# Kernel optimization log

Measured on AMD Instinct MI355X. Metric: run time of the kernel, lower is better.

The kernel has to match this reference:

```python
import jax, jax.numpy as jnp
import numpy as np

N = 64
D_MODEL = 512
L_MAX = 2048
BATCH = 8
DT_MIN, DT_MAX = 1e-3, 1e-1


def _make_s4_buffers(n):
    r = np.arange(1, n + 1, dtype=np.float64)
    # hippo[i,j] = sqrt(2(i+1)+1)*sqrt(2(j+1)+1) if i>j, (i+1)+1 on diag, else 0
    hippo = np.where(r[:, None] > r[None, :],
                     np.sqrt(2 * r[:, None] + 1.0) * np.sqrt(2 * r[None, :] + 1.0),
                     0.0)
    hippo = hippo + np.diag(r + 1.0)
    nhippo = -hippo
    p = 0.5 * np.sqrt(2.0 * r + 1.0)
    q = 2.0 * p
    S = nhippo + p[:, None] * q[None, :]
    lmbda, V = np.linalg.eig(S)
    Vc = V.conj().T
    p = Vc @ p
    q = Vc @ q.conj()
    return (p.astype(np.complex64), q.astype(np.complex64), lmbda.astype(np.complex64))


def setup_inputs() -> dict:
    key = jax.random.key(0)
    ku, kb, kc, ks = jax.random.split(key, 4)
    u = jax.random.normal(ku, (BATCH, L_MAX, D_MODEL), dtype=jnp.float32)
    std = float(np.sqrt(2.0 / (N + D_MODEL)))  # xavier_normal for (n, d_model)
    B = jax.random.normal(kb, (D_MODEL, N), dtype=jnp.float32) * std
    Ct = jax.random.normal(kc, (D_MODEL, N), dtype=jnp.float32) * std
    D = jnp.ones((D_MODEL,), dtype=jnp.float32)
    scale = float(np.log(DT_MAX) - np.log(DT_MIN))
    log_step = jax.random.uniform(ks, (D_MODEL,), dtype=jnp.float32) * scale + float(np.log(DT_MIN))
    p, q, lmbda = _make_s4_buffers(N)
    omega_l = np.exp(2j * np.pi / L_MAX * np.arange(L_MAX)).astype(np.complex64)
    return {"u": u, "B": B, "Ct": Ct, "D": D, "log_step": log_step,
            "p": jnp.asarray(p), "q": jnp.asarray(q), "lmbda": jnp.asarray(lmbda),
            "omega_l": jnp.asarray(omega_l)}


def _s4_kernel(B, Ct, log_step, p, q, lmbda, omega_l):
    L = omega_l.shape[0]
    step = jnp.exp(log_step)                                   # [d]
    g = jnp.outer(2.0 / step, (1.0 - omega_l) / (1.0 + omega_l))  # [d, L] complex
    c = 2.0 / (1.0 + omega_l)                                  # [L]
    # shared Cauchy resolvent: 1/(g - lambda), [d, L, n]
    r = 1.0 / (g[:, :, None] - lmbda)
    a0 = jnp.conj(Ct)  # [d, n]
    a1 = jnp.conj(q)   # [n]
    k00 = jnp.einsum('dn,dln->dl', a0 * B, r)
    k01 = jnp.einsum('dn,dln->dl', a0 * p, r)
    k10 = jnp.einsum('dn,dln->dl', a1 * B, r)
    k11 = jnp.einsum('n,dln->dl', a1 * p, r)
    at_roots = c * (k00 - k01 * (1.0 / (1.0 + k11)) * k10)     # [d, L]
    Kf = jnp.fft.ifft(at_roots, n=L, axis=-1)
    order = (-jnp.arange(L)) % L                               # [0, L-1, ..., 1]
    return Kf[:, order].real                                   # [d, L] float32


def reference(u, B, Ct, D, log_step, p, q, lmbda, omega_l):
    L = u.shape[1]
    K = _s4_kernel(B, Ct, log_step, p, q, lmbda, omega_l)      # [d, L]
    # non-circular FFT convolution
    ud = jnp.fft.rfft(jnp.pad(u, ((0, 0), (0, L), (0, 0))), axis=1)   # [B, L+1, d]
    Kd = jnp.fft.rfft(jnp.pad(K, ((0, 0), (0, L))), axis=-1)          # [d, L+1]
    y = jnp.fft.irfft(ud.transpose(0, 2, 1) * Kd, axis=-1)[..., :L]   # [B, d, L]
    return y.transpose(0, 2, 1) + D[None, None, :] * u
```

## Files before the change

### kernel.cpp

```cpp
#include <hip/hip_runtime.h>
#include <hip/hip_bf16.h>

#define NT 256
#define R2f 0.70710678118654752f
#define CS1 0.92387953251128674f
#define SN1 0.38268343236508978f
#define PI2 6.2831853071795865f

__device__ __forceinline__ float2 cmulf(float2 a, float2 b) {
    return make_float2(a.x * b.x - a.y * b.y, a.x * b.y + a.y * b.x);
}
__device__ __forceinline__ float2 cadd(float2 a, float2 b) { return make_float2(a.x + b.x, a.y + b.y); }
__device__ __forceinline__ float2 csub(float2 a, float2 b) { return make_float2(a.x - b.x, a.y - b.y); }

template<bool INV>
__device__ __forceinline__ float2 tww(float2 v, float wx, float wy) {
    float sy = INV ? -wy : wy;
    return make_float2(v.x * wx - v.y * sy, v.x * sy + v.y * wx);
}
template<bool INV>
__device__ __forceinline__ float2 mul_mi(float2 v) {
    return INV ? make_float2(-v.y, v.x) : make_float2(v.y, -v.x);
}

template<bool INV>
__device__ __forceinline__ void dft4(float2& a, float2& b, float2& c, float2& d) {
    float2 t0 = cadd(a, c), t1 = csub(a, c);
    float2 t2 = cadd(b, d), t3 = csub(b, d);
    float2 jt3 = mul_mi<INV>(t3);
    a = cadd(t0, t2);
    c = csub(t0, t2);
    b = cadd(t1, jt3);
    d = csub(t1, jt3);
}

template<bool INV>
__device__ __forceinline__ void fft16_tail(float2 v[16]) {
    v[5]  = tww<INV>(v[5],  CS1, -SN1);
    v[9]  = tww<INV>(v[9],  R2f, -R2f);
    v[13] = tww<INV>(v[13], SN1, -CS1);
    v[6]  = tww<INV>(v[6],  R2f, -R2f);
    v[10] = mul_mi<INV>(v[10]);
    v[14] = tww<INV>(v[14], -R2f, -R2f);
    v[7]  = tww<INV>(v[7],  SN1, -CS1);
    v[11] = tww<INV>(v[11], -R2f, -R2f);
    v[15] = tww<INV>(v[15], -CS1,  SN1);
    dft4<INV>(v[0],  v[1],  v[2],  v[3]);
    dft4<INV>(v[4],  v[5],  v[6],  v[7]);
    dft4<INV>(v[8],  v[9],  v[10], v[11]);
    dft4<INV>(v[12], v[13], v[14], v[15]);
    float2 t;
    t = v[1];  v[1]  = v[4];  v[4]  = t;
    t = v[2];  v[2]  = v[8];  v[8]  = t;
    t = v[3];  v[3]  = v[12]; v[12] = t;
    t = v[6];  v[6]  = v[9];  v[9]  = t;
    t = v[7];  v[7]  = v[13]; v[13] = t;
    t = v[11]; v[11] = v[14]; v[14] = t;
}

template<bool INV>
__device__ __forceinline__ void fft16(float2 v[16]) {
    dft4<INV>(v[0], v[4], v[8],  v[12]);
    dft4<INV>(v[1], v[5], v[9],  v[13]);
    dft4<INV>(v[2], v[6], v[10], v[14]);
    dft4<INV>(v[3], v[7], v[11], v[15]);
    fft16_tail<INV>(v);
}

__device__ __forceinline__ void fft16_hz(float2 v[16]) {
    #pragma unroll
    for (int i = 0; i < 4; ++i) {
        float2 a = v[i], b = v[i + 4];
        float2 jb = make_float2(b.y, -b.x);
        v[i]      = cadd(a, b);
        v[i + 4]  = cadd(a, jb);
        v[i + 8]  = csub(a, b);
        v[i + 12] = csub(a, jb);
    }
    fft16_tail<false>(v);
}

template<bool INV>
__device__ __forceinline__ void twchain(float2 v[16], float ang) {
    float s, c;
    __sincosf(INV ? ang : -ang, &s, &c);
    float2 w = make_float2(c, s);
    float2 t = w;
    v[1] = cmulf(v[1], t);
    #pragma unroll
    for (int a = 2; a < 16; ++a) { t = cmulf(t, w); v[a] = cmulf(v[a], t); }
}

template<bool INV>
__device__ void fft4096(float2 v[16], float2* lds, int tid) {
    const int hi = tid >> 4, lo = tid & 15;
    if (!INV) {
        fft16_hz(v);
        twchain<false>(v, PI2 * (float)tid * (1.0f / 4096.0f));
        __syncthreads();
        #pragma unroll
        for (int a = 0; a < 16; ++a) lds[tid + 256 * a] = v[a];
        __syncthreads();
        #pragma unroll
        for (int m1 = 0; m1 < 16; ++m1) v[m1] = lds[(m1 * 16 + lo) + 256 * hi];
        fft16<false>(v);
        twchain<false>(v, PI2 * (float)lo * (1.0f / 256.0f));
        __syncthreads();
        #pragma unroll
        for (int b = 0; b < 16; ++b) { int e = lo + 16 * b + 256 * hi; lds[e ^ b] = v[b]; }
        __syncthreads();
        #pragma unroll
        for (int m0 = 0; m0 < 16; ++m0) { int e = m0 + 16 * lo + 256 * hi; v[m0] = lds[e ^ lo]; }
        fft16<false>(v);
    } else {
        fft16<true>(v);
        __syncthreads();
        #pragma unroll
        for (int m0 = 0; m0 < 16; ++m0) { int e = m0 + 16 * lo + 256 * hi; lds[e ^ lo] = v[m0]; }
        __syncthreads();
        #pragma unroll
        for (int b = 0; b < 16; ++b) { int e = lo + 16 * b + 256 * hi; v[b] = lds[e ^ b]; }
        twchain<true>(v, PI2 * (float)lo * (1.0f / 256.0f));
        fft16<true>(v);
        __syncthreads();
        #pragma unroll
        for (int m1 = 0; m1 < 16; ++m1) lds[(m1 * 16 + lo) + 256 * hi] = v[m1];
        __syncthreads();
        #pragma unroll
        for (int a = 0; a < 16; ++a) v[a] = lds[tid + 256 * a];
        twchain<true>(v, PI2 * (float)tid * (1.0f / 4096.0f));
        fft16<true>(v);
    }
}

__global__ __launch_bounds__(256) void cauchy_kernel(
    const float* __restrict__ Bmat, const float* __restrict__ Ct,
    const float* __restrict__ log_step,
    const float2* __restrict__ p, const float2* __restrict__ q,
    const float2* __restrict__ lmbda, const float2* __restrict__ omega,
    float2* __restrict__ at)
{
    __shared__ float4 wA[64];
    __shared__ float4 wB[64];
    const int tid = threadIdx.x;
    const int d = blockIdx.x >> 2;
    const int lbase = (blockIdx.x & 3) << 8;

    if (tid < 64) {
        float b  = Bmat[d * 64 + tid];
        float ct = Ct[d * 64 + tid];
        float2 pp = p[tid], qq = q[tid];
        float2 lam = lmbda[tid];
        wA[tid] = make_float4(lam.x, lam.y, ct * b, qq.x * pp.x + qq.y * pp.y);
        wB[tid] = make_float4(ct * pp.x, ct * pp.y, b * qq.x, b * qq.y);
    }
    __syncthreads();

    const float two_over_dt = 2.0f * __expf(-log_step[d]);
    float2* atd = at + ((size_t)d << 11);

    const int l = lbase + tid;
    float2 om = omega[l];
    float dnx = 1.0f + om.x, dny = om.y;
    float id2 = __builtin_amdgcn_rcpf(dnx * dnx + dny * dny);
    float ivx = dnx * id2, ivy = -dny * id2;
    float ccx = 2.0f * ivx, ccy = 2.0f * ivy;
    float nmx = 1.0f - om.x, nmy = -om.y;
    float gx = two_over_dt * (nmx * ivx - nmy * ivy);
    float gy = two_over_dt * (nmx * ivy + nmy * ivx);

    float S00x = 0.f, S00y = 0.f, Sax = 0.f, Say = 0.f, Sbx = 0.f, Sby = 0.f;
    float Scx = 0.f, Scy = 0.f, Sdx = 0.f, Sdy = 0.f, S11x = 0.f, S11y = 0.f;

    #pragma unroll 8
    for (int n = 0; n < 64; ++n) {
        float4 A  = wA[n];
        float4 Bw = wB[n];
        float dx  = gx - A.x;
        float dy  = gy - A.y;
        float ir  = __builtin_amdgcn_rcpf(fmaf(dx, dx, dy * dy));
        float rx  = dx * ir;
        float ry  = -dy * ir;
        S00x = fmaf(A.z,  rx, S00x); S00y = fmaf(A.z,  ry, S00y);
        S11x = fmaf(A.w,  rx, S11x); S11y = fmaf(A.w,  ry, S11y);
        Sax  = fmaf(Bw.x, rx, Sax);  Say  = fmaf(Bw.x, ry, Say);
        Sbx  = fmaf(Bw.y, rx, Sbx);  Sby  = fmaf(Bw.y, ry, Sby);
        Scx  = fmaf(Bw.z, rx, Scx);  Scy  = fmaf(Bw.z, ry, Scy);
        Sdx  = fmaf(Bw.w, rx, Sdx);  Sdy  = fmaf(Bw.w, ry, Sdy);
    }

    {
        float k01x = Sax - Sby, k01y = Say + Sbx;
        float k10x = Scx + Sdy, k10y = Scy - Sdx;
        float ntx = k01x * k10x - k01y * k10y;
        float nty = k01x * k10y + k01y * k10x;
        float ox = 1.0f + S11x, oy = S11y;
        float oid = __builtin_amdgcn_rcpf(ox * ox + oy * oy);
        float tx = (ntx * ox + nty * oy) * oid;
        float ty = (nty * ox - ntx * oy) * oid;
        float inx = S00x - tx, iny = S00y - ty;
        float2 val = make_float2(ccx * inx - ccy * iny, ccx * iny + ccy * inx);
        atd[l] = val;
        if (l != 0) atd[2048 - l] = make_float2(val.x, -val.y);
    }

    if ((blockIdx.x & 3) == 3 && tid == 0) {
        float2 om1 = omega[1024];
        float dnx1 = 1.0f + om1.x, dny1 = om1.y;
        float id21 = __builtin_amdgcn_rcpf(dnx1 * dnx1 + dny1 * dny1);
        float ivx1 = dnx1 * id21, ivy1 = -dny1 * id21;
        float cx = 2.0f * ivx1, cy = 2.0f * ivy1;
        float nmx1 = 1.0f - om1.x, nmy1 = -om1.y;
        float ggx = two_over_dt * (nmx1 * ivx1 - nmy1 * ivy1);
        float ggy = two_over_dt * (nmx1 * ivy1 + nmy1 * ivx1);
        float s00x = 0.f, s00y = 0.f, sax = 0.f, say = 0.f, sbx = 0.f, sby = 0.f;
        float scx = 0.f, scy = 0.f, sdx = 0.f, sdy = 0.f, s11x = 0.f, s11y = 0.f;
        for (int n = 0; n < 64; ++n) {
            float4 A  = wA[n];
            float4 Bw = wB[n];
            float dx  = ggx - A.x;
            float dy  = ggy - A.y;
            float ir  = __builtin_amdgcn_rcpf(fmaf(dx, dx, dy * dy));
            float rx  = dx * ir;
            float ry  = -dy * ir;
            s00x = fmaf(A.z,  rx, s00x); s00y = fmaf(A.z,  ry, s00y);
            s11x = fmaf(A.w,  rx, s11x); s11y = fmaf(A.w,  ry, s11y);
            sax  = fmaf(Bw.x, rx, sax);  say  = fmaf(Bw.x, ry, say);
            sbx  = fmaf(Bw.y, rx, sbx);  sby  = fmaf(Bw.y, ry, sby);
            scx  = fmaf(Bw.z, rx, scx);  scy  = fmaf(Bw.z, ry, scy);
            sdx  = fmaf(Bw.w, rx, sdx);  sdy  = fmaf(Bw.w, ry, sdy);
        }
        float k01x = sax - sby, k01y = say + sbx;
        float k10x = scx + sdy, k10y = scy - sdx;
        float ntx = k01x * k10x - k01y * k10y;
        float nty = k01x * k10y + k01y * k10x;
        float ox = 1.0f + s11x, oy = s11y;
        float oid = __builtin_amdgcn_rcpf(ox * ox + oy * oy);
        float tx = (ntx * ox + nty * oy) * oid;
        float ty = (nty * ox - ntx * oy) * oid;
        float inx = s00x - tx, iny = s00y - ty;
        atd[1024] = make_float2(cx * inx - cy * iny, cx * iny + cy * inx);
    }
}

__global__ __launch_bounds__(256) void transpose_pack_kernel(
    const float* __restrict__ u, float2* __restrict__ z)
{
    __shared__ float2 tile[64][33];
    const int tid = threadIdx.x;
    int sub = blockIdx.x;
    int lt = sub & 63;
    int dt = (sub >> 6) & 7;
    int bp = sub >> 9;
    const size_t ub0 = (size_t)(2 * bp) * 2048 * 512;
    const size_t ub1 = (size_t)(2 * bp + 1) * 2048 * 512;
    #pragma unroll
    for (int r = 0; r < 8; ++r) {
        int idx = tid + 256 * r;
        int l_in = idx >> 6;
        int d_in = idx & 63;
        size_t off = (size_t)(lt * 32 + l_in) * 512 + (dt * 64 + d_in);
        tile[d_in][l_in] = make_float2(u[ub0 + off], u[ub1 + off]);
    }
    __syncthreads();
    #pragma unroll
    for (int r = 0; r < 8; ++r) {
        int idx = tid + 256 * r;
        int d_out = idx >> 5;
        int l_out = idx & 31;
        z[((size_t)(bp * 512 + dt * 64 + d_out)) * 2048 + lt * 32 + l_out] = tile[d_out][l_out];
    }
}

__global__ __launch_bounds__(256) void khat_kernel(
    const float2* __restrict__ at, float2* __restrict__ Khat)
{
    __shared__ float2 lds[4096];
    const int tid = threadIdx.x;
    const int d = blockIdx.x;
    const int hi = tid >> 4, lo = tid & 15;
    float2 v[16];

    const float2* ap = at + ((size_t)d << 11);
    #pragma unroll
    for (int n2 = 0; n2 < 8; ++n2) v[n2] = ap[tid + 256 * n2];
    #pragma unroll
    for (int n2 = 8; n2 < 16; ++n2) v[n2] = make_float2(0.f, 0.f);

    fft4096<false>(v, lds, tid);

    float* ldsf = (float*)lds;
    __syncthreads();
    if (!(hi & 1)) {
        int a2 = hi >> 1;
        #pragma unroll
        for (int c = 0; c < 16; ++c) {
            int j = 128 * c + 8 * lo + a2;
            ldsf[j ^ ((j >> 5) & 3)] = v[c].x * (1.0f / (2048.0f * 4096.0f));
        }
    }
    __syncthreads();
    #pragma unroll
    for (int n2 = 0; n2 < 8; ++n2) {
        int j = tid + 256 * n2;
        v[n2] = make_float2(ldsf[j ^ ((j >> 5) & 3)], 0.f);
    }
    #pragma unroll
    for (int n2 = 8; n2 < 16; ++n2) v[n2] = make_float2(0.f, 0.f);

    fft4096<false>(v, lds, tid);

    float2* op = Khat + ((size_t)d << 12);
    #pragma unroll
    for (int c = 0; c < 16; ++c) op[c * 256 + tid] = v[c];
}

__global__ __launch_bounds__(256) void conv_kernel(
    float2* __restrict__ z, const float2* __restrict__ Khat,
    const float* __restrict__ D)
{
    __shared__ float2 lds[4096];
    const int tid = threadIdx.x;
    const int d  = blockIdx.x & 511;
    const int bp = blockIdx.x >> 9;
    float2 v[16];
    float2 u0[8];

    float2* zr = z + ((size_t)(bp * 512 + d)) * 2048;
    #pragma unroll
    for (int n2 = 0; n2 < 8; ++n2) { u0[n2] = zr[tid + 256 * n2]; v[n2] = u0[n2]; }
    #pragma unroll
    for (int n2 = 8; n2 < 16; ++n2) v[n2] = make_float2(0.f, 0.f);

    fft4096<false>(v, lds, tid);

    const float2* kh = Khat + ((size_t)d << 12);
    #pragma unroll
    for (int c = 0; c < 16; ++c) v[c] = cmulf(v[c], kh[c * 256 + tid]);

    fft4096<true>(v, lds, tid);

    const float Dd = D[d];
    #pragma unroll
    for (int n2 = 0; n2 < 8; ++n2) {
        zr[tid + 256 * n2] =
            make_float2(v[n2].x + Dd * u0[n2].x, v[n2].y + Dd * u0[n2].y);
    }
}

__global__ __launch_bounds__(256) void untranspose_kernel(
    const float2* __restrict__ yz, float* __restrict__ out)
{
    __shared__ float2 tile[64][65];
    int blk = blockIdx.x;
    int lt  = blk & 31;
    int dt8 = (blk >> 5) & 7;
    int bp  = blk >> 8;
    for (int r = 0; r < 16; ++r) {
        int idx = threadIdx.x + 256 * r;
        int row = idx >> 6;
        int col = idx & 63;
        float2 vv = yz[((size_t)(bp * 512 + dt8 * 64 + row)) * 2048 + lt * 64 + col];
        tile[col][row] = vv;
    }
    __syncthreads();
    const size_t ub0 = (size_t)(2 * bp) * 2048 * 512;
    const size_t ub1 = (size_t)(2 * bp + 1) * 2048 * 512;
    for (int r = 0; r < 16; ++r) {
        int idx = threadIdx.x + 256 * r;
        int row = idx >> 6;
        int col = idx & 63;
        size_t off = (size_t)(lt * 64 + row) * 512 + (dt8 * 64 + col);
        float2 vv = tile[row][col];
        out[ub0 + off] = vv.x;
        out[ub1 + off] = vv.y;
    }
}

extern "C" void kernel_launch(void* const* d_in, const int* in_sizes, int n_in,
                              void* d_out, int out_size, void* d_ws, size_t ws_size,
                              hipStream_t stream) {
    (void)in_sizes; (void)n_in; (void)out_size; (void)ws_size;
    const float*  u   = (const float*)d_in[0];
    const float*  Bm  = (const float*)d_in[1];
    const float*  Ct  = (const float*)d_in[2];
    const float*  D   = (const float*)d_in[3];
    const float*  ls  = (const float*)d_in[4];
    const float2* p   = (const float2*)d_in[5];
    const float2* q   = (const float2*)d_in[6];
    const float2* lm  = (const float2*)d_in[7];
    const float2* om  = (const float2*)d_in[8];
    float* out = (float*)d_out;

    float2* Khat = (float2*)d_ws;
    float2* z    = (float2*)((char*)d_ws + (size_t)512 * 4096 * 8);
    float2* at   = z;

    hipLaunchKernelGGL(cauchy_kernel, dim3(2048), dim3(256), 0, stream,
                       Bm, Ct, ls, p, q, lm, om, at);
    hipLaunchKernelGGL(khat_kernel, dim3(512), dim3(256), 0, stream, at, Khat);
    hipLaunchKernelGGL(transpose_pack_kernel, dim3(2048), dim3(256), 0, stream, u, z);
    hipLaunchKernelGGL(conv_kernel, dim3(2048), dim3(256), 0, stream, z, Khat, D);
    hipLaunchKernelGGL(untranspose_kernel, dim3(1024), dim3(256), 0, stream, z, out);
}
```

Baseline: 93.64 us.

## Split FFT LDS exchanges into real/imag passes with padding to shrink shared memory

The 4096-point FFT now stages data through LDS as separate real and imaginary float passes in a padded float buffer (about 17 KB instead of 32 KB). This roughly halves per-block LDS so more conv blocks can be resident per CU, and padding is meant to cut bank conflicts. The khat kernel is restructured into 1024-thread blocks that each handle four d channels with their own LDS slices. The cost is twice as many __syncthreads and LDS round trips per transpose, and block-wide barriers in khat now span four independent FFTs.

```diff
diff --git a/kernel.cpp b/kernel.cpp
--- a/kernel.cpp
+++ b/kernel.cpp
@@ -6,12 +6,14 @@
 #define CS1 0.92387953251128674f
 #define SN1 0.38268343236508978f
 #define PI2 6.2831853071795865f
+#define LDSN 4336
 
 __device__ __forceinline__ float2 cmulf(float2 a, float2 b) {
     return make_float2(a.x * b.x - a.y * b.y, a.x * b.y + a.y * b.x);
 }
 __device__ __forceinline__ float2 cadd(float2 a, float2 b) { return make_float2(a.x + b.x, a.y + b.y); }
 __device__ __forceinline__ float2 csub(float2 a, float2 b) { return make_float2(a.x - b.x, a.y - b.y); }
+__device__ __forceinline__ int padx(int i) { return i + ((i >> 8) << 4); }
 
 template<bool INV>
 __device__ __forceinline__ float2 tww(float2 v, float wx, float wy) {
@@ -92,42 +94,66 @@
 }
 
 template<bool INV>
-__device__ void fft4096(float2 v[16], float2* lds, int tid) {
+__device__ void fft4096(float2 v[16], float* ldsf, int tid) {
     const int hi = tid >> 4, lo = tid & 15;
     if (!INV) {
         fft16_hz(v);
         twchain<false>(v, PI2 * (float)tid * (1.0f / 4096.0f));
         __syncthreads();
         #pragma unroll
-        for (int a = 0; a < 16; ++a) lds[tid + 256 * a] = v[a];
-        __syncthreads();
-        #pragma unroll
-        for (int m1 = 0; m1 < 16; ++m1) v[m1] = lds[(m1 * 16 + lo) + 256 * hi];
+        for (int a = 0; a < 16; ++a) ldsf[padx(tid + 256 * a)] = v[a].x;
+        __syncthreads();
+        #pragma unroll
+        for (int m1 = 0; m1 < 16; ++m1) v[m1].x = ldsf[padx(m1 * 16 + lo + 256 * hi)];
+        __syncthreads();
+        #pragma unroll
+        for (int a = 0; a < 16; ++a) ldsf[padx(tid + 256 * a)] = v[a].y;
+        __syncthreads();
+        #pragma unroll
+        for (int m1 = 0; m1 < 16; ++m1) v[m1].y = ldsf[padx(m1 * 16 + lo + 256 * hi)];
         fft16<false>(v);
         twchain<false>(v, PI2 * (float)lo * (1.0f / 256.0f));
         __syncthreads();
         #pragma unroll
-        for (int b = 0; b < 16; ++b) { int e = lo + 16 * b + 256 * hi; lds[e ^ b] = v[b]; }
-        __syncthreads();
-        #pragma unroll
-        for (int m0 = 0; m0 < 16; ++m0) { int e = m0 + 16 * lo + 256 * hi; v[m0] = lds[e ^ lo]; }
+        for (int b = 0; b < 16; ++b) ldsf[padx((lo + 16 * b + 256 * hi) ^ b)] = v[b].x;
+        __syncthreads();
+        #pragma unroll
+        for (int m0 = 0; m0 < 16; ++m0) v[m0].x = ldsf[padx((m0 + 16 * lo + 256 * hi) ^ lo)];
+        __syncthreads();
+        #pragma unroll
+        for (int b = 0; b < 16; ++b) ldsf[padx((lo + 16 * b + 256 * hi) ^ b)] = v[b].y;
+        __syncthreads();
+        #pragma unroll
+        for (int m0 = 0; m0 < 16; ++m0) v[m0].y = ldsf[padx((m0 + 16 * lo + 256 * hi) ^ lo)];
         fft16<false>(v);
     } else {
         fft16<true>(v);
         __syncthreads();
         #pragma unroll
-        for (int m0 = 0; m0 < 16; ++m0) { int e = m0 + 16 * lo + 256 * hi; lds[e ^ lo] = v[m0]; }
-        __syncthreads();
-        #pragma unroll
-        for (int b = 0; b < 16; ++b) { int e = lo + 16 * b + 256 * hi; v[b] = lds[e ^ b]; }
+        for (int m0 = 0; m0 < 16; ++m0) ldsf[padx((m0 + 16 * lo + 256 * hi) ^ lo)] = v[m0].x;
+        __syncthreads();
+        #pragma unroll
+        for (int b = 0; b < 16; ++b) v[b].x = ldsf[padx((lo + 16 * b + 256 * hi) ^ b)];
+        __syncthreads();
+        #pragma unroll
+        for (int m0 = 0; m0 < 16; ++m0) ldsf[padx((m0 + 16 * lo + 256 * hi) ^ lo)] = v[m0].y;
+        __syncthreads();
+        #pragma unroll
+        for (int b = 0; b < 16; ++b) v[b].y = ldsf[padx((lo + 16 * b + 256 * hi) ^ b)];
         twchain<true>(v, PI2 * (float)lo * (1.0f / 256.0f));
         fft16<true>(v);
         __syncthreads();
         #pragma unroll
-        for (int m1 = 0; m1 < 16; ++m1) lds[(m1 * 16 + lo) + 256 * hi] = v[m1];
-        __syncthreads();
-        #pragma unroll
-        for (int a = 0; a < 16; ++a) v[a] = lds[tid + 256 * a];
+        for (int m1 = 0; m1 < 16; ++m1) ldsf[padx(m1 * 16 + lo + 256 * hi)] = v[m1].x;
+        __syncthreads();
+        #pragma unroll
+        for (int a = 0; a < 16; ++a) v[a].x = ldsf[padx(tid + 256 * a)];
+        __syncthreads();
+        #pragma unroll
+        for (int m1 = 0; m1 < 16; ++m1) ldsf[padx(m1 * 16 + lo + 256 * hi)] = v[m1].y;
+        __syncthreads();
+        #pragma unroll
+        for (int a = 0; a < 16; ++a) v[a].y = ldsf[padx(tid + 256 * a)];
         twchain<true>(v, PI2 * (float)tid * (1.0f / 4096.0f));
         fft16<true>(v);
     }
@@ -243,6 +269,50 @@
     }
 }
 
+__global__ __launch_bounds__(1024) void khat_kernel(
+    const float2* __restrict__ at, float2* __restrict__ Khat)
+{
+    __shared__ float ldsf[4 * LDSN];
+    const int sub = threadIdx.x & 255;
+    const int grp = threadIdx.x >> 8;
+    const int d = (blockIdx.x << 2) | grp;
+    float* lf = ldsf + grp * LDSN;
+    const int hi = sub >> 4, lo = sub & 15;
+    float2 v[16];
+
+    const float2* ap = at + ((size_t)d << 11);
+    #pragma unroll
+    for (int n2 = 0; n2 < 8; ++n2) v[n2] = ap[sub + 256 * n2];
+    #pragma unroll
+    for (int n2 = 8; n2 < 16; ++n2) v[n2] = make_float2(0.f, 0.f);
+
+    fft4096<false>(v, lf, sub);
+
+    __syncthreads();
+    if (!(hi & 1)) {
+        int a2 = hi >> 1;
+        #pragma unroll
+        for (int c = 0; c < 16; ++c) {
+            int j = 128 * c + 8 * lo + a2;
+            lf[j ^ ((j >> 5) & 3)] = v[c].x * (1.0f / (2048.0f * 4096.0f));
+        }
+    }
+    __syncthreads();
+    #pragma unroll
+    for (int n2 = 0; n2 < 8; ++n2) {
+        int j = sub + 256 * n2;
+        v[n2] = make_float2(lf[j ^ ((j >> 5) & 3)], 0.f);
+    }
+    #pragma unroll
+    for (int n2 = 8; n2 < 16; ++n2) v[n2] = make_float2(0.f, 0.f);
+
+    fft4096<false>(v, lf, sub);
+
+    float2* op = Khat + ((size_t)d << 12);
+    #pragma unroll
+    for (int c = 0; c < 16; ++c) op[c * 256 + sub] = v[c];
+}
+
 __global__ __launch_bounds__(256) void transpose_pack_kernel(
     const float* __restrict__ u, float2* __restrict__ z)
 {
@@ -272,54 +342,11 @@
     }
 }
 
-__global__ __launch_bounds__(256) void khat_kernel(
-    const float2* __restrict__ at, float2* __restrict__ Khat)
-{
-    __shared__ float2 lds[4096];
-    const int tid = threadIdx.x;
-    const int d = blockIdx.x;
-    const int hi = tid >> 4, lo = tid & 15;
-    float2 v[16];
-
-    const float2* ap = at + ((size_t)d << 11);
-    #pragma unroll
-    for (int n2 = 0; n2 < 8; ++n2) v[n2] = ap[tid + 256 * n2];
-    #pragma unroll
-    for (int n2 = 8; n2 < 16; ++n2) v[n2] = make_float2(0.f, 0.f);
-
-    fft4096<false>(v, lds, tid);
-
-    float* ldsf = (float*)lds;
-    __syncthreads();
-    if (!(hi & 1)) {
-        int a2 = hi >> 1;
-        #pragma unroll
-        for (int c = 0; c < 16; ++c) {
-            int j = 128 * c + 8 * lo + a2;
-            ldsf[j ^ ((j >> 5) & 3)] = v[c].x * (1.0f / (2048.0f * 4096.0f));
-        }
-    }
-    __syncthreads();
-    #pragma unroll
-    for (int n2 = 0; n2 < 8; ++n2) {
-        int j = tid + 256 * n2;
-        v[n2] = make_float2(ldsf[j ^ ((j >> 5) & 3)], 0.f);
-    }
-    #pragma unroll
-    for (int n2 = 8; n2 < 16; ++n2) v[n2] = make_float2(0.f, 0.f);
-
-    fft4096<false>(v, lds, tid);
-
-    float2* op = Khat + ((size_t)d << 12);
-    #pragma unroll
-    for (int c = 0; c < 16; ++c) op[c * 256 + tid] = v[c];
-}
-
 __global__ __launch_bounds__(256) void conv_kernel(
     float2* __restrict__ z, const float2* __restrict__ Khat,
     const float* __restrict__ D)
 {
-    __shared__ float2 lds[4096];
+    __shared__ float ldsf[LDSN];
     const int tid = threadIdx.x;
     const int d  = blockIdx.x & 511;
     const int bp = blockIdx.x >> 9;
@@ -332,13 +359,13 @@
     #pragma unroll
     for (int n2 = 8; n2 < 16; ++n2) v[n2] = make_float2(0.f, 0.f);
 
-    fft4096<false>(v, lds, tid);
+    fft4096<false>(v, ldsf, tid);
 
     const float2* kh = Khat + ((size_t)d << 12);
     #pragma unroll
     for (int c = 0; c < 16; ++c) v[c] = cmulf(v[c], kh[c * 256 + tid]);
 
-    fft4096<true>(v, lds, tid);
+    fft4096<true>(v, ldsf, tid);
 
     const float Dd = D[d];
     #pragma unroll
@@ -398,7 +425,7 @@
 
     hipLaunchKernelGGL(cauchy_kernel, dim3(2048), dim3(256), 0, stream,
                        Bm, Ct, ls, p, q, lm, om, at);
-    hipLaunchKernelGGL(khat_kernel, dim3(512), dim3(256), 0, stream, at, Khat);
+    hipLaunchKernelGGL(khat_kernel, dim3(128), dim3(1024), 0, stream, at, Khat);
     hipLaunchKernelGGL(transpose_pack_kernel, dim3(2048), dim3(256), 0, stream, u, z);
     hipLaunchKernelGGL(conv_kernel, dim3(2048), dim3(256), 0, stream, z, Khat, D);
     hipLaunchKernelGGL(untranspose_kernel, dim3(1024), dim3(256), 0, stream, z, out);
```

Measured after the change: 100.8 us. +7.6%, slower.
